# Performance work log

Hardware: AMD Instinct MI355X
Metric: run time of the kernel (lower is better)

The kernel has to match this reference:

```python
import jax, jax.numpy as jnp
import numpy as np

NUM_EMBEDDINGS = 8192
EMBEDDING_DIM = 64
COMMITMENT_COST = 0.25


def setup_inputs() -> dict:
    key = jax.random.key(0)
    kx, ke = jax.random.split(key)
    x = jax.random.normal(kx, (32, 1024, EMBEDDING_DIM), dtype=jnp.float32)
    embeddings = jax.random.normal(ke, (NUM_EMBEDDINGS, EMBEDDING_DIM), dtype=jnp.float32)
    return {"x": x, "embeddings": embeddings}


def reference(x, embeddings):
    d = embeddings.shape[1]
    flat_x = x.reshape(-1, d)  # [N, D]
    # squared euclidean distances (argmin identical to cdist argmin):
    d2 = (
        jnp.sum(flat_x * flat_x, axis=-1, keepdims=True)
        - 2.0 * flat_x @ embeddings.T
        + jnp.sum(embeddings * embeddings, axis=-1)
    )
    encoding_indices = jnp.argmin(d2, axis=1)  # [N]
    quantized = embeddings[encoding_indices].reshape(x.shape)
    codebook_loss = jnp.mean((jax.lax.stop_gradient(quantized) - x) ** 2)
    commitment_loss = COMMITMENT_COST * jnp.mean((quantized - jax.lax.stop_gradient(x)) ** 2)
    loss = codebook_loss + commitment_loss
    # straight-through estimator
    quantized_st = x + jax.lax.stop_gradient(quantized - x)
    return quantized_st, loss, encoding_indices
```

## Files before the change

kernel.cpp:

```cpp
#include <hip/hip_runtime.h>
#include <hip/hip_bf16.h>
#include <float.h>

#define N_ROWS 32768
#define DIMS   64
#define K_EMB  8192
#define NT     (K_EMB / 16)
#define NQ     8
#define NTQ    (NT / NQ)
#define RG     4
#define KEYMASK 0xFFFFFFC0u
#define GAP_THR 3.5e-3f

typedef __attribute__((ext_vector_type(8))) short s8v;
typedef __attribute__((ext_vector_type(4))) float f4v;
typedef __attribute__((ext_vector_type(4))) int   i4v;

#define WS_EFRAG 0
#define WS_EN2   (2 * 1024 * 1024)
#define WS_IDX   (WS_EN2 + K_EMB * 4)
#define WS_KEY   (WS_IDX + N_ROWS * 4)
#define WS_BH    (WS_KEY + N_ROWS * 8)
#define WS_SH    (WS_BH + NQ * N_ROWS * 4)
#define WS_CH    (WS_SH + NQ * N_ROWS * 4)
#define WS_CTL   (WS_CH + NQ * N_ROWS * 4)
#define WS_WL    (WS_CTL + 16)

#define OUT_LOSS (N_ROWS * DIMS)
#define OUT_IDX  (N_ROWS * DIMS + 1)

__device__ inline short bfh(float v) {
    __hip_bfloat16 h = __float2bfloat16(v);
    return __builtin_bit_cast(short, h);
}
__device__ inline float bff(short s) {
    __hip_bfloat16 h = __builtin_bit_cast(__hip_bfloat16, s);
    return __bfloat162float(h);
}

__global__ void vq_prep(const float* __restrict__ emb, short* __restrict__ efrag,
                        float* __restrict__ en2, int4* __restrict__ ctl) {
    if (blockIdx.x == 0 && threadIdx.x == 0) *ctl = make_int4(0, 0, 0, 0);
    int gid = blockIdx.x * 128 + threadIdx.x;
    int t = gid >> 6, lane = gid & 63;
    int m = lane & 15, q = lane >> 4;
    const float* er = emb + (size_t)(t * 16 + m) * DIMS;
    s8v hi0, lo0, hi1, lo1;
    float ss = 0.f;
#pragma unroll
    for (int j = 0; j < 8; ++j) {
        float v0 = er[q * 8 + j];
        float v1 = er[32 + q * 8 + j];
        ss += v0 * v0 + v1 * v1;
        short h0 = bfh(v0); lo0[j] = bfh(v0 - bff(h0)); hi0[j] = h0;
        short h1 = bfh(v1); lo1[j] = bfh(v1 - bff(h1)); hi1[j] = h1;
    }
    s8v* base = (s8v*)efrag + (size_t)t * 4 * 64;
    base[0 * 64 + lane] = hi0;
    base[1 * 64 + lane] = hi1;
    base[2 * 64 + lane] = lo0;
    base[3 * 64 + lane] = lo1;
    ss += __shfl_xor(ss, 16, 64);
    ss += __shfl_xor(ss, 32, 64);
    if (q == 0) en2[t * 16 + m] = -0.5f * ss;
}

#define LOADT(B0, B1, B2, B3, CC, T) do {                 \
    const i4v* _p = bsrc + (size_t)(T) * 256;             \
    B0 = _p[lane];       B1 = _p[64 + lane];              \
    B2 = _p[128 + lane]; B3 = _p[192 + lane];             \
    CC = ep[(T) * 16];                                    \
} while (0)

#define COMPT(B0, B1, B2, B3, CC, CODE) do {                                     \
    f4v cinit = {CC, CC, CC, CC};                 \
    _Pragma("unroll")                                                            \
    for (int g = 0; g < RG; ++g) {                                               \
        f4v acc;                                                                 \
        acc = __builtin_amdgcn_mfma_f32_16x16x32_bf16(ahi[g][0], __builtin_bit_cast(s8v, B0), cinit, 0, 0, 0); \
        acc = __builtin_amdgcn_mfma_f32_16x16x32_bf16(ahi[g][1], __builtin_bit_cast(s8v, B1), acc, 0, 0, 0);   \
        acc = __builtin_amdgcn_mfma_f32_16x16x32_bf16(ahi[g][0], __builtin_bit_cast(s8v, B2), acc, 0, 0, 0);   \
        acc = __builtin_amdgcn_mfma_f32_16x16x32_bf16(ahi[g][1], __builtin_bit_cast(s8v, B3), acc, 0, 0, 0);   \
        acc = __builtin_amdgcn_mfma_f32_16x16x32_bf16(alo[g][0], __builtin_bit_cast(s8v, B0), acc, 0, 0, 0);   \
        acc = __builtin_amdgcn_mfma_f32_16x16x32_bf16(alo[g][1], __builtin_bit_cast(s8v, B1), acc, 0, 0, 0);   \
        _Pragma("unroll")                                                        \
        for (int r = 0; r < 4; ++r) {        \
            float kf = __uint_as_float(                                          \
                (__float_as_uint(acc[r]) & KEYMASK) | (unsigned)(CODE));         \
            sec[g][r]  = __builtin_amdgcn_fmed3f(kf, sec[g][r], best[g][r]);     \
            best[g][r] = fmaxf(best[g][r], kf);                                  \
        }                                                                        \
    }                                                                            \
} while (0)

__global__ __launch_bounds__(64)
__attribute__((amdgpu_waves_per_eu(2, 3))) void vq_phase1(
    const float* __restrict__ x, const short* __restrict__ efrag,
    const float* __restrict__ en2,
    float* __restrict__ bh, float* __restrict__ sh, int* __restrict__ ch) {
    int lane = threadIdx.x;
    int m = lane & 15, q = lane >> 4;
    int kh = blockIdx.y;
    int row0 = blockIdx.x * 64;

    s8v ahi[RG][2], alo[RG][2];
#pragma unroll
    for (int g = 0; g < RG; ++g) {
        const float* xr = x + (size_t)(row0 + g * 16 + m) * DIMS + q * 8;
#pragma unroll
        for (int j = 0; j < 8; ++j) {
            float v0 = xr[j], v1 = xr[32 + j];
            short h0 = bfh(v0); alo[g][0][j] = bfh(v0 - bff(h0)); ahi[g][0][j] = h0;
            short h1 = bfh(v1); alo[g][1][j] = bfh(v1 - bff(h1)); ahi[g][1][j] = h1;
        }
    }

    float best[RG][4], sec[RG][4];
#pragma unroll
    for (int g = 0; g < RG; ++g)
#pragma unroll
        for (int r = 0; r < 4; ++r) { best[g][r] = -FLT_MAX; sec[g][r] = -FLT_MAX; }

    const i4v*   bsrc = (const i4v*)efrag + (size_t)kh * NTQ * 256;
    const float* ep   = en2 + (size_t)kh * NTQ * 16 + m;

    i4v A0, A1, A2, A3, B0, B1, B2, B3;
    float cA, cB;
    LOADT(A0, A1, A2, A3, cA, 0);
#pragma unroll 1
    for (int t = 0; t < NTQ; t += 2) {
        LOADT(B0, B1, B2, B3, cB, t + 1);
        COMPT(A0, A1, A2, A3, cA, t);
        if (t + 2 < NTQ) LOADT(A0, A1, A2, A3, cA, t + 2);
        COMPT(B0, B1, B2, B3, cB, t + 1);
    }

#pragma unroll
    for (int g = 0; g < RG; ++g)
#pragma unroll
    for (int r = 0; r < 4; ++r) {
        float b = best[g][r], sv = sec[g][r];
#pragma unroll
        for (int off = 1; off < 16; off <<= 1) {
            float ob = __shfl_xor(b, off, 64);
            float os = __shfl_xor(sv, off, 64);
            sv = fmaxf(fminf(b, ob), fmaxf(sv, os));
            b  = fmaxf(b, ob);
        }
        unsigned long long bal =
            __ballot(__float_as_uint(best[g][r]) == __float_as_uint(b));
        int win = __ffsll(bal >> (q * 16)) - 1;
        if (m == win) {
            int tl  = (int)(__float_as_uint(b) & 63u);
            int col = ((kh * NTQ + tl) << 4) | m;
            int o = kh * N_ROWS + row0 + g * 16 + q * 4 + r;
            bh[o] = b; sh[o] = sv; ch[o] = col;
        }
    }
}

__global__ void vq_merge(const float* __restrict__ bh, const float* __restrict__ sh,
                         const int* __restrict__ ch, int* __restrict__ idx_buf,
                         unsigned long long* __restrict__ key8,
                         float* __restrict__ nbv,
                         int* __restrict__ wl, int* __restrict__ wl_count) {
    int row = blockIdx.x * 256 + threadIdx.x;
    float nb = bh[row];
    int   c  = ch[row];
    float ns = -FLT_MAX;
#pragma unroll
    for (int h = 1; h < NQ; ++h) {
        float b = bh[h * N_ROWS + row];
        int   cc = ch[h * N_ROWS + row];
        if (b > nb) { ns = nb; nb = b; c = cc; }
        else        { ns = fmaxf(ns, b); }
    }
#pragma unroll
    for (int h = 0; h < NQ; ++h) ns = fmaxf(ns, sh[h * N_ROWS + row]);
    idx_buf[row] = c;
    key8[row] = 0ULL;
    nbv[row] = nb;
    if (nb - ns < GAP_THR) {
        int pos = atomicAdd(wl_count, 1);
        wl[pos] = row;
    }
}

__global__ __launch_bounds__(64) void vq_fixup(
    const float* __restrict__ x, const float* __restrict__ emb,
    const float* __restrict__ en2, const float* __restrict__ nbv,
    unsigned long long* __restrict__ key8,
    const int* __restrict__ wl, const int* __restrict__ wl_count) {
    int lane = threadIdx.x;
    int cchunk = blockIdx.x & 127;
    int rslice = blockIdx.x >> 7;
    int cnt = *wl_count;
    if (rslice >= cnt) return;
    int c = cchunk * 64 + lane;
    const float4* er = (const float4*)(emb + (size_t)c * DIMS);
    float4 e[16];
#pragma unroll
    for (int qq = 0; qq < 16; ++qq) e[qq] = er[qq];
    float c0 = en2[c];
    for (int wi = rslice; wi < cnt; wi += 16) {
        int row = wl[wi];
        const float4* xr = (const float4*)(x + (size_t)row * DIMS);
        float d = 0.f;
#pragma unroll
        for (int qq = 0; qq < 16; ++qq) {
            float4 ee = e[qq];
            float4 xx = xr[qq];
            d += ee.x * xx.x + ee.y * xx.y + ee.z * xx.z + ee.w * xx.w;
        }
        float bf_ = d + c0;
        int bc_ = c;
#pragma unroll
        for (int off = 1; off < 64; off <<= 1) {
            float of = __shfl_xor(bf_, off, 64);
            int   oc = __shfl_xor(bc_, off, 64);
            if (of > bf_ || (of == bf_ && oc < bc_)) { bf_ = of; bc_ = oc; }
        }
        if (lane == 0 && bf_ >= nbv[row] - GAP_THR) {
            unsigned int u = __float_as_uint(bf_);
            unsigned int sb = ((int)u < 0) ? ~u : (u | 0x80000000u);
            unsigned long long key = ((unsigned long long)sb << 32) | (unsigned int)(~bc_);
            atomicMax(&key8[row], key);
        }
    }
}

__global__ void vq_gather(const float* __restrict__ x, const float* __restrict__ emb,
                          const int* __restrict__ idx_buf,
                          const unsigned long long* __restrict__ key8,
                          float* __restrict__ out, double* __restrict__ loss_acc,
                          int* __restrict__ done_count) {
    int row = blockIdx.x * blockDim.x + threadIdx.x;
    unsigned long long k = key8[row];
    int idx = k ? (int)(~(unsigned int)k) : idx_buf[row];
    const float4* ev = (const float4*)(emb + (size_t)idx * DIMS);
    const float4* xv = (const float4*)(x + (size_t)row * DIMS);
    float4* ov = (float4*)(out + (size_t)row * DIMS);
    float s = 0.f;
#pragma unroll
    for (int qq = 0; qq < 16; ++qq) {
        float4 ee = ev[qq];
        float4 xx = xv[qq];
        float dx = ee.x - xx.x, dy = ee.y - xx.y, dz = ee.z - xx.z, dw = ee.w - xx.w;
        s += dx * dx + dy * dy + dz * dz + dw * dw;
        ov[qq] = ee;
    }
#pragma unroll
    for (int off = 32; off > 0; off >>= 1) s += __shfl_down(s, off, 64);
    if ((threadIdx.x & 63) == 0) atomicAdd(loss_acc, (double)s);
    out[OUT_IDX + row] = (float)idx;
    __syncthreads();
    if (threadIdx.x == 0) {
        __threadfence();
        int d = atomicAdd(done_count, 1);
        if (d == (int)gridDim.x - 1) {
            double total = atomicAdd(loss_acc, 0.0);
            out[OUT_LOSS] = (float)(1.25 * total / (double)(N_ROWS * DIMS));
        }
    }
}

extern "C" void kernel_launch(void* const* d_in, const int* in_sizes, int n_in,
                              void* d_out, int out_size, void* d_ws, size_t ws_size,
                              hipStream_t stream) {
    const float* x   = (const float*)d_in[0];
    const float* emb = (const float*)d_in[1];
    float* out = (float*)d_out;
    char*  ws  = (char*)d_ws;

    short* efrag   = (short*)(ws + WS_EFRAG);
    float* en2     = (float*)(ws + WS_EN2);
    int*   idx_buf = (int*)(ws + WS_IDX);
    unsigned long long* key8 = (unsigned long long*)(ws + WS_KEY);
    float* bhb     = (float*)(ws + WS_BH);
    float* shb     = (float*)(ws + WS_SH);
    int*   chb     = (int*)(ws + WS_CH);
    double* loss_acc = (double*)(ws + WS_CTL);
    int*   wl_count  = (int*)(ws + WS_CTL + 8);
    int*   done_cnt  = (int*)(ws + WS_CTL + 12);
    int*   wl        = (int*)(ws + WS_WL);

    vq_prep<<<(NT * 64) / 128, 128, 0, stream>>>(emb, efrag, en2, (int4*)(ws + WS_CTL));
    vq_phase1<<<dim3(N_ROWS / 64, NQ), 64, 0, stream>>>(x, efrag, en2, bhb, shb, chb);
    vq_merge<<<N_ROWS / 256, 256, 0, stream>>>(bhb, shb, chb, idx_buf, key8, bhb, wl, wl_count);
    vq_fixup<<<2048, 64, 0, stream>>>(x, emb, en2, bhb, key8, wl, wl_count);
    vq_gather<<<N_ROWS / 256, 256, 0, stream>>>(x, emb, idx_buf, key8, out, loss_acc, done_cnt);
}
```

Baseline: 193.4 us.

## Split codebook into 16 chunks and interleave MFMA chains across row groups

Doubles the number of codebook partitions in the distance phase from 8 to 16. The grid gets twice as many blocks and each block scans half as many tiles, so the tile-code field in the packed key shrinks from 6 to 5 bits, which keeps one more mantissa bit. The MFMA sequence is reordered so the four row groups' accumulation chains interleave instead of running back to back, hiding MFMA dependency latency. The merge output now goes to a separate nbv buffer instead of overwriting bh, since bh now holds 16 partitions. Merge has to reduce twice as many partial results per row, adding some merge work and memory traffic.

```diff
diff --git a/kernel.cpp b/kernel.cpp
--- a/kernel.cpp
+++ b/kernel.cpp
@@ -6,10 +6,10 @@
 #define DIMS   64
 #define K_EMB  8192
 #define NT     (K_EMB / 16)
-#define NQ     8
+#define NQ     16
 #define NTQ    (NT / NQ)
 #define RG     4
-#define KEYMASK 0xFFFFFFC0u
+#define KEYMASK 0xFFFFFFE0u
 #define GAP_THR 3.5e-3f
 
 typedef __attribute__((ext_vector_type(8))) short s8v;
@@ -23,9 +23,9 @@
 #define WS_BH    (WS_KEY + N_ROWS * 8)
 #define WS_SH    (WS_BH + NQ * N_ROWS * 4)
 #define WS_CH    (WS_SH + NQ * N_ROWS * 4)
-#define WS_CTL   (WS_CH + NQ * N_ROWS * 4)
+#define WS_NBV   (WS_CH + NQ * N_ROWS * 4)
+#define WS_CTL   (WS_NBV + N_ROWS * 4)
 #define WS_WL    (WS_CTL + 16)
-
 #define OUT_LOSS (N_ROWS * DIMS)
 #define OUT_IDX  (N_ROWS * DIMS + 1)
 
@@ -72,25 +72,35 @@
     CC = ep[(T) * 16];                                    \
 } while (0)
 
+#define MF(AF, BB, CI) __builtin_amdgcn_mfma_f32_16x16x32_bf16(AF, __builtin_bit_cast(s8v, BB), CI, 0, 0, 0)
+
+#define KEYUP(AG, G, CODE) do {                                                  \
+    _Pragma("unroll")                                                            \
+    for (int r = 0; r < 4; ++r) {            \
+        float kf = __uint_as_float(                                              \
+            (__float_as_uint(AG[r]) & KEYMASK) | (unsigned)(CODE));              \
+        sec[G][r]  = __builtin_amdgcn_fmed3f(kf, sec[G][r], best[G][r]);         \
+        best[G][r] = fmaxf(best[G][r], kf);                                      \
+    }                                                                            \
+} while (0)
+
 #define COMPT(B0, B1, B2, B3, CC, CODE) do {                                     \
     f4v cinit = {CC, CC, CC, CC};                 \
-    _Pragma("unroll")                                                            \
-    for (int g = 0; g < RG; ++g) {                                               \
-        f4v acc;                                                                 \
-        acc = __builtin_amdgcn_mfma_f32_16x16x32_bf16(ahi[g][0], __builtin_bit_cast(s8v, B0), cinit, 0, 0, 0); \
-        acc = __builtin_amdgcn_mfma_f32_16x16x32_bf16(ahi[g][1], __builtin_bit_cast(s8v, B1), acc, 0, 0, 0);   \
-        acc = __builtin_amdgcn_mfma_f32_16x16x32_bf16(ahi[g][0], __builtin_bit_cast(s8v, B2), acc, 0, 0, 0);   \
-        acc = __builtin_amdgcn_mfma_f32_16x16x32_bf16(ahi[g][1], __builtin_bit_cast(s8v, B3), acc, 0, 0, 0);   \
-        acc = __builtin_amdgcn_mfma_f32_16x16x32_bf16(alo[g][0], __builtin_bit_cast(s8v, B0), acc, 0, 0, 0);   \
-        acc = __builtin_amdgcn_mfma_f32_16x16x32_bf16(alo[g][1], __builtin_bit_cast(s8v, B1), acc, 0, 0, 0);   \
-        _Pragma("unroll")                                                        \
-        for (int r = 0; r < 4; ++r) {        \
-            float kf = __uint_as_float(                                          \
-                (__float_as_uint(acc[r]) & KEYMASK) | (unsigned)(CODE));         \
-            sec[g][r]  = __builtin_amdgcn_fmed3f(kf, sec[g][r], best[g][r]);     \
-            best[g][r] = fmaxf(best[g][r], kf);                                  \
-        }                                                                        \
-    }                                                                            \
+    f4v a0, a1, a2, a3;                                                          \
+    a0 = MF(ahi[0][0], B0, cinit); a1 = MF(ahi[1][0], B0, cinit);                \
+    a2 = MF(ahi[2][0], B0, cinit); a3 = MF(ahi[3][0], B0, cinit);                \
+    a0 = MF(ahi[0][1], B1, a0); a1 = MF(ahi[1][1], B1, a1);                      \
+    a2 = MF(ahi[2][1], B1, a2); a3 = MF(ahi[3][1], B1, a3);                      \
+    a0 = MF(ahi[0][0], B2, a0); a1 = MF(ahi[1][0], B2, a1);                      \
+    a2 = MF(ahi[2][0], B2, a2); a3 = MF(ahi[3][0], B2, a3);                      \
+    a0 = MF(ahi[0][1], B3, a0); a1 = MF(ahi[1][1], B3, a1);                      \
+    a2 = MF(ahi[2][1], B3, a2); a3 = MF(ahi[3][1], B3, a3);                      \
+    a0 = MF(alo[0][0], B0, a0); a1 = MF(alo[1][0], B0, a1);                      \
+    a2 = MF(alo[2][0], B0, a2); a3 = MF(alo[3][0], B0, a3);                      \
+    a0 = MF(alo[0][1], B1, a0); a1 = MF(alo[1][1], B1, a1);                      \
+    a2 = MF(alo[2][1], B1, a2); a3 = MF(alo[3][1], B1, a3);                      \
+    KEYUP(a0, 0, CODE); KEYUP(a1, 1, CODE);                                      \
+    KEYUP(a2, 2, CODE); KEYUP(a3, 3, CODE);                                      \
 } while (0)
 
 __global__ __launch_bounds__(64)
@@ -151,7 +161,7 @@
             __ballot(__float_as_uint(best[g][r]) == __float_as_uint(b));
         int win = __ffsll(bal >> (q * 16)) - 1;
         if (m == win) {
-            int tl  = (int)(__float_as_uint(b) & 63u);
+            int tl  = (int)(__float_as_uint(b) & 31u);
             int col = ((kh * NTQ + tl) << 4) | m;
             int o = kh * N_ROWS + row0 + g * 16 + q * 4 + r;
             bh[o] = b; sh[o] = sv; ch[o] = col;
@@ -279,6 +289,7 @@
     float* bhb     = (float*)(ws + WS_BH);
     float* shb     = (float*)(ws + WS_SH);
     int*   chb     = (int*)(ws + WS_CH);
+    float* nbv     = (float*)(ws + WS_NBV);
     double* loss_acc = (double*)(ws + WS_CTL);
     int*   wl_count  = (int*)(ws + WS_CTL + 8);
     int*   done_cnt  = (int*)(ws + WS_CTL + 12);
@@ -286,7 +297,7 @@
 
     vq_prep<<<(NT * 64) / 128, 128, 0, stream>>>(emb, efrag, en2, (int4*)(ws + WS_CTL));
     vq_phase1<<<dim3(N_ROWS / 64, NQ), 64, 0, stream>>>(x, efrag, en2, bhb, shb, chb);
-    vq_merge<<<N_ROWS / 256, 256, 0, stream>>>(bhb, shb, chb, idx_buf, key8, bhb, wl, wl_count);
-    vq_fixup<<<2048, 64, 0, stream>>>(x, emb, en2, bhb, key8, wl, wl_count);
+    vq_merge<<<N_ROWS / 256, 256, 0, stream>>>(bhb, shb, chb, idx_buf, key8, nbv, wl, wl_count);
+    vq_fixup<<<2048, 64, 0, stream>>>(x, emb, en2, nbv, key8, wl, wl_count);
     vq_gather<<<N_ROWS / 256, 256, 0, stream>>>(x, emb, idx_buf, key8, out, loss_acc, done_cnt);
 }
```

Result: slower. 198.5 us (+2.7%).
